# Performance work log

Measured on AMD Instinct MI355X. Metric: run time of the kernel, lower is better.

The kernel has to match this reference:

```python
import jax, jax.numpy as jnp
import numpy as np

B, N, T, C, H = 64, 17, 512, 64, 4
DK = C // H  # 16
EPS = 1e-5  # BatchNorm eps (eval mode: running_mean=0, running_var=1)


def setup_inputs() -> dict:
    ks = jax.random.split(jax.random.key(0), 10)
    x = jax.random.normal(ks[0], (B, N, T, C), dtype=jnp.float32)
    adj = jax.random.randint(ks[1], (B, N, N), 0, 2).astype(jnp.int32)
    W = jax.random.normal(ks[2], (C, C), dtype=jnp.float32) * 0.1   # Linear(in_ch, out_ch) weight [out, in]
    a = jax.random.normal(ks[3], (1, 2 * DK), dtype=jnp.float32) * 0.1  # Linear(2*d_k, 1) weight
    w1 = jax.random.normal(ks[4], (C, 1, 3), dtype=jnp.float32) * 0.3  # depthwise conv [C,1,k]
    gamma1 = jax.random.uniform(ks[5], (C,), dtype=jnp.float32)
    beta1 = jax.random.normal(ks[6], (C,), dtype=jnp.float32) * 0.1
    w2 = jax.random.normal(ks[7], (C, 1, 3), dtype=jnp.float32) * 0.3
    gamma2 = jax.random.uniform(ks[8], (C,), dtype=jnp.float32)
    beta2 = jax.random.normal(ks[9], (C,), dtype=jnp.float32) * 0.1
    return {"x": x, "adj": adj, "W": W, "a": a, "w1": w1, "gamma1": gamma1,
            "beta1": beta1, "w2": w2, "gamma2": gamma2, "beta2": beta2}


def _depth_tcn(x, w, gamma, beta, dilation):
    """x: [B*N, C, T] -> causal depthwise conv (k=3) + eval-BN + GELU."""
    pad = 2 * dilation  # (k-1)*dilation
    xp = jnp.pad(x, ((0, 0), (0, 0), (pad, 0)))
    y = jax.lax.conv_general_dilated(
        xp, w, window_strides=(1,), padding='VALID', rhs_dilation=(dilation,),
        dimension_numbers=('NCH', 'OIH', 'NCH'), feature_group_count=x.shape[1])
    # BatchNorm1d in eval: running_mean=0, running_var=1
    y = y / jnp.sqrt(1.0 + EPS) * gamma[None, :, None] + beta[None, :, None]
    return jax.nn.gelu(y, approximate=False)


def _forward(x, W, a, w1, gamma1, beta1, w2, gamma2, beta2, adj):
    Bv, Nv, Tv, Cv = x.shape
    BT = Bv * Tv
    # ---- GAT ----
    h0 = x.transpose(0, 2, 1, 3).reshape(BT, Nv, Cv)          # [BT,N,C]
    h = jnp.einsum('bnc,oc->bno', h0, W).reshape(BT, Nv, H, DK)
    # a @ cat(h_i, h_j) == h_i . a[:DK] + h_j . a[DK:]  (exact decomposition,
    # avoids materializing the [BT,N,N,H,2*DK] concat tensor)
    s = jnp.einsum('bnhd,d->bnh', h, a[0, :DK])               # source term
    t = jnp.einsum('bnhd,d->bnh', h, a[0, DK:])               # target term
    e = jax.nn.leaky_relu(s[:, :, None, :] + t[:, None, :, :], 0.2)  # [BT,i,j,H]
    adj_bt = jnp.broadcast_to(adj[:, None, :, :], (Bv, Tv, Nv, Nv)).reshape(BT, Nv, Nv)
    bias = jnp.where(adj_bt == 0, jnp.float32(-1e9), jnp.float32(0.0))[..., None]
    alpha = jax.nn.softmax(e + bias, axis=2)                  # softmax over j
    # faithful to torch einsum 'btnh,bnhd->bnhd' (sums alpha over first node axis)
    scale = alpha.sum(axis=1)                                 # [BT, N, H]
    g = (h * scale[..., None]).reshape(BT, Nv, Cv) + h0       # residual inside GAT
    # ---- TCN (reshape sequence replicated literally from the torch code) ----
    g = g.reshape(Bv, Tv, Nv, Cv).transpose(0, 2, 1, 3)       # [B,N,T,C]
    g = g.reshape(Bv * Nv, Cv, Tv)                            # (interleaves T/C, as in torch)
    g = _depth_tcn(g, w1, gamma1, beta1, 1)
    g = _depth_tcn(g, w2, gamma2, beta2, 2)
    g = g.reshape(Bv, Nv, Cv, Tv).transpose(0, 1, 3, 2)       # [B,N,T,C]
    # ---- residual path (Identity since in_ch == hid_ch, reshapes replicated) ----
    res = x.transpose(0, 3, 1, 2).reshape(Bv * Nv, Cv, Tv)
    res = res.reshape(Bv, Nv, Cv, Tv).transpose(0, 1, 3, 2)
    return g + res


def reference(x, adj, W, a, w1, gamma1, beta1, w2, gamma2, beta2):
    return _forward(x, W, a, w1, gamma1, beta1, w2, gamma2, beta2, adj)
```

## Files before the change

### kernel.cpp

```cpp
#include <hip/hip_runtime.h>
#include <math.h>

typedef float f32x4 __attribute__((ext_vector_type(4)));

#define SLAB 32768
#define BSLAB 557056

__device__ __forceinline__ float gelu_exact(float x) {
  return 0.5f * x * (1.0f + erff(x * 0.7071067811865475f));
}

__global__ __launch_bounds__(256) void k_gatgemm(const float* __restrict__ X,
                                                 const float* __restrict__ W,
                                                 const int* __restrict__ adj,
                                                 const float* __restrict__ avec,
                                                 float* __restrict__ g,
                                                 float* __restrict__ resP) {
  const int tid = threadIdx.x;
  const int lane = tid & 63, wv = tid >> 6;
  const int b = blockIdx.x >> 7;
  const int t = ((blockIdx.x & 127) << 2) | wv;

  __shared__ float xsA[4][17 * 68];
  __shared__ float hsA[4][17 * 68];
  __shared__ float smA[4][272];
  __shared__ float scA[4][68];
  __shared__ float av[32];
  __shared__ int adjs[289];

  float* xs = xsA[wv];
  float* hs = hsA[wv];
  float* sv = smA[wv];
  float* tv = sv + 68;
  float* mrow = sv + 136;
  float* sinv = sv + 204;
  float* scalev = scA[wv];

  const long base = (long)b * BSLAB + (long)t * 64;

  if (tid < 32) av[tid] = avec[tid];
  for (int idx = tid; idx < 289; idx += 256) adjs[idx] = adj[b * 289 + idx];

  float xr[17];
#pragma unroll
  for (int n = 0; n < 17; ++n) xr[n] = X[base + (long)n * SLAB + lane];

  f32x4 wr[16];
  {
    const float* wrow = W + lane * 64;
#pragma unroll
    for (int k = 0; k < 16; ++k) wr[k] = *(const f32x4*)(wrow + k * 4);
  }

#pragma unroll
  for (int n = 0; n < 17; ++n) xs[n * 68 + lane] = xr[n];

  __syncthreads();

#pragma unroll
  for (int n = 0; n < 17; ++n) {
    float acc = 0.f;
#pragma unroll
    for (int c4 = 0; c4 < 16; ++c4) {
      f32x4 xv = *(const f32x4*)(xs + n * 68 + c4 * 4);
      acc = fmaf(xv.x, wr[c4].x, acc);
      acc = fmaf(xv.y, wr[c4].y, acc);
      acc = fmaf(xv.z, wr[c4].z, acc);
      acc = fmaf(xv.w, wr[c4].w, acc);
    }
    hs[n * 68 + lane] = acc;
  }

#pragma unroll
  for (int it = 0; it < 2; ++it) {
    int item = lane + it * 64;
    if (item < 68) {
      int n = item >> 2, h = item & 3;
      float s = 0.f, tt = 0.f;
#pragma unroll
      for (int d = 0; d < 16; ++d) {
        float hv = hs[n * 68 + h * 16 + d];
        s += hv * av[d];
        tt += hv * av[16 + d];
      }
      sv[item] = s;
      tv[item] = tt;
    }
  }

#pragma unroll
  for (int it = 0; it < 2; ++it) {
    int item = lane + it * 64;
    if (item < 68) {
      int i = item >> 2, h = item & 3;
      float si = sv[item];
      float e[17];
      float mx = -3.4e38f;
#pragma unroll
      for (int j = 0; j < 17; ++j) {
        float v = si + tv[j * 4 + h];
        v = (v >= 0.f) ? v : 0.2f * v;
        if (adjs[i * 17 + j] == 0) v += -1e9f;
        e[j] = v;
        mx = fmaxf(mx, v);
      }
      float sum = 0.f;
#pragma unroll
      for (int j = 0; j < 17; ++j) sum += expf(e[j] - mx);
      mrow[item] = mx;
      sinv[item] = 1.0f / sum;
    }
  }

#pragma unroll
  for (int it = 0; it < 2; ++it) {
    int item = lane + it * 64;
    if (item < 68) {
      int j = item >> 2, h = item & 3;
      float tj = tv[item];
      float sc = 0.f;
#pragma unroll
      for (int i = 0; i < 17; ++i) {
        float v = sv[i * 4 + h] + tj;
        v = (v >= 0.f) ? v : 0.2f * v;
        if (adjs[i * 17 + j] == 0) v += -1e9f;
        sc += expf(v - mrow[i * 4 + h]) * sinv[i * 4 + h];
      }
      scalev[item] = sc;
    }
  }

#pragma unroll
  for (int n = 0; n < 17; ++n) {
    long a = base + (long)n * SLAB + lane;
    int m = n * 64 + lane;
    g[a] = hs[n * 68 + lane] * scalev[n * 4 + (lane >> 4)] + xs[n * 68 + lane];
    resP[a] = xs[(m % 17) * 68 + (m / 17)];
  }
}

__global__ __launch_bounds__(256) void k_tcn(const float* __restrict__ g,
                                             const float* __restrict__ w1,
                                             const float* __restrict__ gamma1,
                                             const float* __restrict__ beta1,
                                             const float* __restrict__ w2,
                                             const float* __restrict__ gamma2,
                                             const float* __restrict__ beta2,
                                             float* __restrict__ out) {
  const int bn = blockIdx.x;
  const int tid = threadIdx.x;
  const int cc = tid >> 2, q = tid & 3;

  __shared__ float L[64 * 257];

  const long gbase = (long)bn * SLAB + cc * 512;
  const long obase = (long)bn * SLAB;

  const float bnmul = 0.9999950000374997f;
  const float w10 = w1[cc * 3 + 0], w11 = w1[cc * 3 + 1], w12 = w1[cc * 3 + 2];
  const float w20 = w2[cc * 3 + 0], w21 = w2[cc * 3 + 1], w22 = w2[cc * 3 + 2];
  const float bs1 = gamma1[cc] * bnmul, bb1 = beta1[cc];
  const float bs2 = gamma2[cc] * bnmul, bb2 = beta2[cc];

  const int t0 = q * 128;

  for (int h = 0; h < 2; ++h) {
    if ((q >> 1) == h) {
      float gm1 = 0.f, gm2 = 0.f;
      float zm1 = 0.f, zm2 = 0.f, zm3 = 0.f, zm4 = 0.f;
      if (q > 0) {
        float gg[6];
#pragma unroll
        for (int k = 0; k < 6; ++k) gg[k] = g[gbase + (t0 - 6 + k)];
        zm4 = gelu_exact((w10 * gg[0] + w11 * gg[1] + w12 * gg[2]) * bs1 + bb1);
        zm3 = gelu_exact((w10 * gg[1] + w11 * gg[2] + w12 * gg[3]) * bs1 + bb1);
        zm2 = gelu_exact((w10 * gg[2] + w11 * gg[3] + w12 * gg[4]) * bs1 + bb1);
        zm1 = gelu_exact((w10 * gg[3] + w11 * gg[4] + w12 * gg[5]) * bs1 + bb1);
        gm2 = gg[4];
        gm1 = gg[5];
      }
      for (int blk = 0; blk < 32; ++blk) {
        f32x4 gv4 = *(const f32x4*)(g + gbase + t0 + blk * 4);
#pragma unroll
        for (int j = 0; j < 4; ++j) {
          float gv = gv4[j];
          float z = gelu_exact((w10 * gm2 + w11 * gm1 + w12 * gv) * bs1 + bb1);
          float y = gelu_exact((w20 * zm4 + w21 * zm2 + w22 * z) * bs2 + bb2);
          L[cc * 257 + (t0 + blk * 4 + j - h * 256)] = y;
          gm2 = gm1; gm1 = gv;
          zm4 = zm3; zm3 = zm2; zm2 = zm1; zm1 = z;
        }
      }
    }
    __syncthreads();

    for (int k = 0; k < 16; ++k) {
      int f4 = h * 4096 + tid + k * 256;
      int flat = f4 * 4;
      int t = flat >> 6, c0 = flat & 63;
      f32x4 r4 = *(const f32x4*)(out + obase + flat);
      f32x4 o4;
#pragma unroll
      for (int j = 0; j < 4; ++j)
        o4[j] = L[(c0 + j) * 257 + (t - h * 256)] + r4[j];
      *(f32x4*)(out + obase + flat) = o4;
    }
    __syncthreads();
  }
}

extern "C" void kernel_launch(void* const* d_in, const int* in_sizes, int n_in,
                              void* d_out, int out_size, void* d_ws, size_t ws_size,
                              hipStream_t stream) {
  const float* x = (const float*)d_in[0];
  const int* adj = (const int*)d_in[1];
  const float* W = (const float*)d_in[2];
  const float* avec = (const float*)d_in[3];
  const float* w1 = (const float*)d_in[4];
  const float* gamma1 = (const float*)d_in[5];
  const float* beta1 = (const float*)d_in[6];
  const float* w2 = (const float*)d_in[7];
  const float* gamma2 = (const float*)d_in[8];
  const float* beta2 = (const float*)d_in[9];

  float* g = (float*)d_ws;
  float* out = (float*)d_out;

  k_gatgemm<<<8192, 256, 0, stream>>>(x, W, adj, avec, g, out);
  k_tcn<<<1088, 256, 0, stream>>>(g, w1, gamma1, beta1, w2, gamma2, beta2, out);
}
```

Baseline: 551.7 us.

## Split TCN across four blocks per sequence and use fast exp in GAT softmax

The TCN kernel now launches four blocks per (b,n) row, each covering 128 time steps, with each thread handling 32 steps of one channel. Before, a block ran two serialized halves where only half the threads computed at a time. Every thread now computes, and the shared tile is transposed to [t][c] so the residual add can read it vectorized. The cost is extra halo recomputation per thread (six-sample warmup). The GAT softmax also switches expf to __expf, which is cheaper but less accurate.

```diff
diff --git a/kernel.cpp b/kernel.cpp
--- a/kernel.cpp
+++ b/kernel.cpp
@@ -106,7 +106,7 @@
       }
       float sum = 0.f;
 #pragma unroll
-      for (int j = 0; j < 17; ++j) sum += expf(e[j] - mx);
+      for (int j = 0; j < 17; ++j) sum += __expf(e[j] - mx);
       mrow[item] = mx;
       sinv[item] = 1.0f / sum;
     }
@@ -124,7 +124,7 @@
         float v = sv[i * 4 + h] + tj;
         v = (v >= 0.f) ? v : 0.2f * v;
         if (adjs[i * 17 + j] == 0) v += -1e9f;
-        sc += expf(v - mrow[i * 4 + h]) * sinv[i * 4 + h];
+        sc += __expf(v - mrow[i * 4 + h]) * sinv[i * 4 + h];
       }
       scalev[item] = sc;
     }
@@ -147,65 +147,65 @@
                                              const float* __restrict__ gamma2,
                                              const float* __restrict__ beta2,
                                              float* __restrict__ out) {
-  const int bn = blockIdx.x;
+  const int bn = blockIdx.x >> 2;
+  const int Q = blockIdx.x & 3;
   const int tid = threadIdx.x;
-  const int cc = tid >> 2, q = tid & 3;
-
-  __shared__ float L[64 * 257];
-
-  const long gbase = (long)bn * SLAB + cc * 512;
+  const int c = tid & 63;
+  const int sq = tid >> 6;
+
+  __shared__ float L[128 * 68];
+
+  const long gbase = (long)bn * SLAB + c * 512;
   const long obase = (long)bn * SLAB;
 
   const float bnmul = 0.9999950000374997f;
-  const float w10 = w1[cc * 3 + 0], w11 = w1[cc * 3 + 1], w12 = w1[cc * 3 + 2];
-  const float w20 = w2[cc * 3 + 0], w21 = w2[cc * 3 + 1], w22 = w2[cc * 3 + 2];
-  const float bs1 = gamma1[cc] * bnmul, bb1 = beta1[cc];
-  const float bs2 = gamma2[cc] * bnmul, bb2 = beta2[cc];
-
-  const int t0 = q * 128;
-
-  for (int h = 0; h < 2; ++h) {
-    if ((q >> 1) == h) {
-      float gm1 = 0.f, gm2 = 0.f;
-      float zm1 = 0.f, zm2 = 0.f, zm3 = 0.f, zm4 = 0.f;
-      if (q > 0) {
-        float gg[6];
-#pragma unroll
-        for (int k = 0; k < 6; ++k) gg[k] = g[gbase + (t0 - 6 + k)];
-        zm4 = gelu_exact((w10 * gg[0] + w11 * gg[1] + w12 * gg[2]) * bs1 + bb1);
-        zm3 = gelu_exact((w10 * gg[1] + w11 * gg[2] + w12 * gg[3]) * bs1 + bb1);
-        zm2 = gelu_exact((w10 * gg[2] + w11 * gg[3] + w12 * gg[4]) * bs1 + bb1);
-        zm1 = gelu_exact((w10 * gg[3] + w11 * gg[4] + w12 * gg[5]) * bs1 + bb1);
-        gm2 = gg[4];
-        gm1 = gg[5];
-      }
-      for (int blk = 0; blk < 32; ++blk) {
-        f32x4 gv4 = *(const f32x4*)(g + gbase + t0 + blk * 4);
-#pragma unroll
-        for (int j = 0; j < 4; ++j) {
-          float gv = gv4[j];
-          float z = gelu_exact((w10 * gm2 + w11 * gm1 + w12 * gv) * bs1 + bb1);
-          float y = gelu_exact((w20 * zm4 + w21 * zm2 + w22 * z) * bs2 + bb2);
-          L[cc * 257 + (t0 + blk * 4 + j - h * 256)] = y;
-          gm2 = gm1; gm1 = gv;
-          zm4 = zm3; zm3 = zm2; zm2 = zm1; zm1 = z;
-        }
-      }
-    }
-    __syncthreads();
-
-    for (int k = 0; k < 16; ++k) {
-      int f4 = h * 4096 + tid + k * 256;
-      int flat = f4 * 4;
-      int t = flat >> 6, c0 = flat & 63;
-      f32x4 r4 = *(const f32x4*)(out + obase + flat);
-      f32x4 o4;
-#pragma unroll
-      for (int j = 0; j < 4; ++j)
-        o4[j] = L[(c0 + j) * 257 + (t - h * 256)] + r4[j];
-      *(f32x4*)(out + obase + flat) = o4;
-    }
-    __syncthreads();
+  const float w10 = w1[c * 3 + 0], w11 = w1[c * 3 + 1], w12 = w1[c * 3 + 2];
+  const float w20 = w2[c * 3 + 0], w21 = w2[c * 3 + 1], w22 = w2[c * 3 + 2];
+  const float bs1 = gamma1[c] * bnmul, bb1 = beta1[c];
+  const float bs2 = gamma2[c] * bnmul, bb2 = beta2[c];
+
+  const int t0 = Q * 128 + sq * 32;
+  const int tl0 = sq * 32;
+
+  float gm1 = 0.f, gm2 = 0.f;
+  float zm1 = 0.f, zm2 = 0.f, zm3 = 0.f, zm4 = 0.f;
+  if (t0 > 0) {
+    float gg[6];
+#pragma unroll
+    for (int k = 0; k < 6; ++k) gg[k] = g[gbase + (t0 - 6 + k)];
+    zm4 = gelu_exact((w10 * gg[0] + w11 * gg[1] + w12 * gg[2]) * bs1 + bb1);
+    zm3 = gelu_exact((w10 * gg[1] + w11 * gg[2] + w12 * gg[3]) * bs1 + bb1);
+    zm2 = gelu_exact((w10 * gg[2] + w11 * gg[3] + w12 * gg[4]) * bs1 + bb1);
+    zm1 = gelu_exact((w10 * gg[3] + w11 * gg[4] + w12 * gg[5]) * bs1 + bb1);
+    gm2 = gg[4];
+    gm1 = gg[5];
+  }
+
+  for (int blk = 0; blk < 8; ++blk) {
+    f32x4 gv4 = *(const f32x4*)(g + gbase + t0 + blk * 4);
+#pragma unroll
+    for (int j = 0; j < 4; ++j) {
+      float gv = gv4[j];
+      float z = gelu_exact((w10 * gm2 + w11 * gm1 + w12 * gv) * bs1 + bb1);
+      float y = gelu_exact((w20 * zm4 + w21 * zm2 + w22 * z) * bs2 + bb2);
+      L[(tl0 + blk * 4 + j) * 68 + c] = y;
+      gm2 = gm1; gm1 = gv;
+      zm4 = zm3; zm3 = zm2; zm2 = zm1; zm1 = z;
+    }
+  }
+  __syncthreads();
+
+  for (int k = 0; k < 8; ++k) {
+    int f4 = tid + k * 256;
+    int flat = Q * 8192 + f4 * 4;
+    int tl = f4 >> 4;
+    int c0 = (f4 & 15) * 4;
+    f32x4 l4 = *(const f32x4*)(L + tl * 68 + c0);
+    f32x4 r4 = *(const f32x4*)(out + obase + flat);
+    f32x4 o4;
+#pragma unroll
+    for (int j = 0; j < 4; ++j) o4[j] = l4[j] + r4[j];
+    *(f32x4*)(out + obase + flat) = o4;
   }
 }
 
@@ -227,5 +227,5 @@
   float* out = (float*)d_out;
 
   k_gatgemm<<<8192, 256, 0, stream>>>(x, W, adj, avec, g, out);
-  k_tcn<<<1088, 256, 0, stream>>>(g, w1, gamma1, beta1, w2, gamma2, beta2, out);
-}
+  k_tcn<<<4352, 256, 0, stream>>>(g, w1, gamma1, beta1, w2, gamma2, beta2, out);
+}
```

Result: faster. 464.8 us (-15.7%).
